# Performance work log

Hardware: AMD Instinct MI355X
Metric: run time of the kernel (lower is better)

Reference implementation:

```python
import jax, jax.numpy as jnp
import numpy as np

N_NODES = 100000
N_EDGES = 1600000
D_FEAT = 128


def setup_inputs() -> dict:
    key = jax.random.key(0)
    k1, k2, k3 = jax.random.split(key, 3)
    feat = jax.random.normal(k1, (N_NODES, D_FEAT), dtype=jnp.float32)
    src = jax.random.randint(k2, (N_EDGES,), 0, N_NODES, dtype=jnp.int32)
    dst = jax.random.randint(k3, (N_EDGES,), 0, N_NODES, dtype=jnp.int32)
    return {"feat": feat, "src": src, "dst": dst}


def reference(feat, src, dst):
    # DGL update_all(copy_src('h','m'), mean('m','neigh')):
    # gather src features along edges, segment-sum into dst, divide by in-degree.
    msgs = feat[src]  # [E, D] gather
    neigh_sum = jax.ops.segment_sum(msgs, dst, num_segments=N_NODES)  # [N, D]
    deg = jax.ops.segment_sum(jnp.ones((src.shape[0],), dtype=feat.dtype), dst,
                              num_segments=N_NODES)  # [N]
    # DGL mean yields 0 for zero in-degree nodes; clamp denominator to 1.
    h_neigh = neigh_sum / jnp.maximum(deg, 1.0)[:, None]
    return h_neigh
```

## Files before the change

### kernel.cpp

```cpp
#include <hip/hip_runtime.h>

#define N_NODES 100000
#define N_EDGES 1600000
#define D_FEAT  128

#define NBUCK   ((N_NODES + 255) >> 8)
#define CAP     8192


__global__ void k1_coarse_hist(const int* __restrict__ dst,
                               int* __restrict__ ghist) {
    __shared__ int lh[NBUCK];
    for (int t = threadIdx.x; t < NBUCK; t += blockDim.x) lh[t] = 0;
    __syncthreads();
    const size_t total4 = N_EDGES / 4;
    size_t tid    = (size_t)blockIdx.x * blockDim.x + threadIdx.x;
    size_t stride = (size_t)gridDim.x * blockDim.x;
    for (size_t i = tid; i < total4; i += stride) {
        int4 d4 = reinterpret_cast<const int4*>(dst)[i];
        atomicAdd(&lh[d4.x >> 8], 1);
        atomicAdd(&lh[d4.y >> 8], 1);
        atomicAdd(&lh[d4.z >> 8], 1);
        atomicAdd(&lh[d4.w >> 8], 1);
    }
    __syncthreads();
    for (int t = threadIdx.x; t < NBUCK; t += blockDim.x)
        if (lh[t]) atomicAdd(&ghist[t], lh[t]);
}

__global__ void k2_scan(const int* __restrict__ ghist,
                        int* __restrict__ base,
                        int* __restrict__ gcursor) {
    __shared__ int ls[512];
    const int t = threadIdx.x;
    int v = (t < NBUCK) ? ghist[t] : 0;
    ls[t] = v;
    __syncthreads();
    int x = v;
    for (int off = 1; off < 512; off <<= 1) {
        int y = (t >= off) ? ls[t - off] : 0;
        __syncthreads();
        x += y;
        ls[t] = x;
        __syncthreads();
    }
    if (t < NBUCK) {
        base[t]    = x - v;
        gcursor[t] = x - v;
    }
}

__global__ void k3_bucket(const int* __restrict__ src,
                          const int* __restrict__ dst,
                          int* __restrict__ gcursor,
                          int* __restrict__ packed) {
    __shared__ int lh[NBUCK];
    __shared__ int lcur[NBUCK];
    const int total4  = N_EDGES / 4;
    const int chunk4  = (total4 + gridDim.x - 1) / gridDim.x;
    const int start4  = blockIdx.x * chunk4;
    const int end4    = min(total4, start4 + chunk4);

    for (int t = threadIdx.x; t < NBUCK; t += blockDim.x) lh[t] = 0;
    __syncthreads();
    for (int i = start4 + threadIdx.x; i < end4; i += blockDim.x) {
        int4 d4 = reinterpret_cast<const int4*>(dst)[i];
        atomicAdd(&lh[d4.x >> 8], 1);
        atomicAdd(&lh[d4.y >> 8], 1);
        atomicAdd(&lh[d4.z >> 8], 1);
        atomicAdd(&lh[d4.w >> 8], 1);
    }
    __syncthreads();
    for (int t = threadIdx.x; t < NBUCK; t += blockDim.x)
        lcur[t] = lh[t] ? atomicAdd(&gcursor[t], lh[t]) : 0;
    __syncthreads();
    for (int i = start4 + threadIdx.x; i < end4; i += blockDim.x) {
        int4 d4 = reinterpret_cast<const int4*>(dst)[i];
        int4 s4 = reinterpret_cast<const int4*>(src)[i];
        int slot;
        slot = atomicAdd(&lcur[d4.x >> 8], 1);
        packed[slot] = s4.x | ((d4.x & 255) << 17);
        slot = atomicAdd(&lcur[d4.y >> 8], 1);
        packed[slot] = s4.y | ((d4.y & 255) << 17);
        slot = atomicAdd(&lcur[d4.z >> 8], 1);
        packed[slot] = s4.z | ((d4.z & 255) << 17);
        slot = atomicAdd(&lcur[d4.w >> 8], 1);
        packed[slot] = s4.w | ((d4.w & 255) << 17);
    }
}

__global__ void __launch_bounds__(256)
k4_fine(const int* __restrict__ ghist,
        const int* __restrict__ base,
        int* __restrict__ packed,
        int* __restrict__ deg,
        int* __restrict__ offs) {
    __shared__ int lpk[CAP];
    __shared__ int lcnt[256];
    __shared__ int lscan[256];
    __shared__ int lcur[256];
    const int b  = blockIdx.x;
    const int t  = threadIdx.x;
    const int gb = base[b];
    int nb = ghist[b];
    if (nb > CAP) nb = CAP;

    lcnt[t] = 0;
    __syncthreads();
    for (int idx = t; idx < nb; idx += 256) {
        const int p = packed[gb + idx];
        lpk[idx] = p;
        atomicAdd(&lcnt[(p >> 17) & 255], 1);
    }
    __syncthreads();
    lscan[t] = lcnt[t];
    __syncthreads();
    int x = lcnt[t];
    for (int off = 1; off < 256; off <<= 1) {
        int y = (t >= off) ? lscan[t - off] : 0;
        __syncthreads();
        x += y;
        lscan[t] = x;
        __syncthreads();
    }
    const int excl = x - lcnt[t];
    const int node = (b << 8) + t;
    if (node < N_NODES) {
        deg[node]  = lcnt[t];
        offs[node] = gb + excl;
    }
    lcur[t] = excl;
    __syncthreads();
    for (int idx = t; idx < nb; idx += 256) {
        const int p    = lpk[idx];
        const int slot = atomicAdd(&lcur[(p >> 17) & 255], 1);
        packed[gb + slot] = p & 0x1FFFF;
    }
}

__global__ void __launch_bounds__(256)
aggregate(const float* __restrict__ feat,
          const int*   __restrict__ edge_list,
          const int*   __restrict__ offs,
          const int*   __restrict__ deg,
          float*       __restrict__ out) {
    const size_t gtid = (size_t)blockIdx.x * blockDim.x + threadIdx.x;
    const int node = (int)(gtid >> 5);
    const int lane = threadIdx.x & 31;
    if (node >= N_NODES) return;

    const int base = offs[node];
    const int d    = deg[node];
    const size_t col = (size_t)lane * 4;

    float4 acc0 = make_float4(0.f, 0.f, 0.f, 0.f);
    float4 acc1 = make_float4(0.f, 0.f, 0.f, 0.f);
    float4 acc2 = make_float4(0.f, 0.f, 0.f, 0.f);
    float4 acc3 = make_float4(0.f, 0.f, 0.f, 0.f);

    int j = 0;
    for (; j + 3 < d; j += 4) {
        const int s0 = edge_list[base + j];
        const int s1 = edge_list[base + j + 1];
        const int s2 = edge_list[base + j + 2];
        const int s3 = edge_list[base + j + 3];
        float4 a = *reinterpret_cast<const float4*>(feat + (size_t)s0 * D_FEAT + col);
        float4 b = *reinterpret_cast<const float4*>(feat + (size_t)s1 * D_FEAT + col);
        float4 c = *reinterpret_cast<const float4*>(feat + (size_t)s2 * D_FEAT + col);
        float4 e = *reinterpret_cast<const float4*>(feat + (size_t)s3 * D_FEAT + col);
        acc0.x += a.x; acc0.y += a.y; acc0.z += a.z; acc0.w += a.w;
        acc1.x += b.x; acc1.y += b.y; acc1.z += b.z; acc1.w += b.w;
        acc2.x += c.x; acc2.y += c.y; acc2.z += c.z; acc2.w += c.w;
        acc3.x += e.x; acc3.y += e.y; acc3.z += e.z; acc3.w += e.w;
    }
    for (; j < d; ++j) {
        const int s0 = edge_list[base + j];
        float4 a = *reinterpret_cast<const float4*>(feat + (size_t)s0 * D_FEAT + col);
        acc0.x += a.x; acc0.y += a.y; acc0.z += a.z; acc0.w += a.w;
    }
    const float inv = 1.0f / (float)max(d, 1);
    float4 r;
    r.x = (acc0.x + acc1.x + acc2.x + acc3.x) * inv;
    r.y = (acc0.y + acc1.y + acc2.y + acc3.y) * inv;
    r.z = (acc0.z + acc1.z + acc2.z + acc3.z) * inv;
    r.w = (acc0.w + acc1.w + acc2.w + acc3.w) * inv;
    *reinterpret_cast<float4*>(out + (size_t)node * D_FEAT + col) = r;
}

__global__ void zero_out_deg(float* __restrict__ out, float* __restrict__ deg) {
    const size_t total4 = (size_t)N_NODES * D_FEAT / 4;
    size_t tid    = (size_t)blockIdx.x * blockDim.x + threadIdx.x;
    size_t stride = (size_t)gridDim.x * blockDim.x;
    float4 z = make_float4(0.f, 0.f, 0.f, 0.f);
    for (size_t i = tid; i < total4; i += stride)
        reinterpret_cast<float4*>(out)[i] = z;
    for (size_t i = tid; i < N_NODES; i += stride)
        deg[i] = 0.f;
}

__global__ void scatter_atomic(const float* __restrict__ feat,
                               const int*   __restrict__ src,
                               const int*   __restrict__ dst,
                               float*       __restrict__ out,
                               float*       __restrict__ deg) {
    const size_t total  = (size_t)N_EDGES * 32;
    size_t tid    = (size_t)blockIdx.x * blockDim.x + threadIdx.x;
    size_t stride = (size_t)gridDim.x * blockDim.x;
    for (size_t i = tid; i < total; i += stride) {
        const int e = (int)(i >> 5);
        const int c = (int)(i & 31);
        const int s = src[e];
        const int d = dst[e];
        float4 v = reinterpret_cast<const float4*>(feat + (size_t)s * D_FEAT)[c];
        float* o = out + (size_t)d * D_FEAT + (size_t)c * 4;
        unsafeAtomicAdd(o + 0, v.x);
        unsafeAtomicAdd(o + 1, v.y);
        unsafeAtomicAdd(o + 2, v.z);
        unsafeAtomicAdd(o + 3, v.w);
        if (c == 0) unsafeAtomicAdd(deg + d, 1.0f);
    }
}

__global__ void div_mean(float* __restrict__ out, const float* __restrict__ deg) {
    const size_t total4 = (size_t)N_NODES * D_FEAT / 4;
    size_t tid    = (size_t)blockIdx.x * blockDim.x + threadIdx.x;
    size_t stride = (size_t)gridDim.x * blockDim.x;
    for (size_t i = tid; i < total4; i += stride) {
        const float inv = 1.0f / fmaxf(deg[i >> 5], 1.0f);
        float4 v = reinterpret_cast<float4*>(out)[i];
        v.x *= inv; v.y *= inv; v.z *= inv; v.w *= inv;
        reinterpret_cast<float4*>(out)[i] = v;
    }
}

extern "C" void kernel_launch(void* const* d_in, const int* in_sizes, int n_in,
                              void* d_out, int out_size, void* d_ws, size_t ws_size,
                              hipStream_t stream) {
    const float* feat = (const float*)d_in[0];
    const int*   src  = (const int*)d_in[1];
    const int*   dst  = (const int*)d_in[2];
    float* out = (float*)d_out;

    const size_t need = ((size_t)1536 + 2 * N_NODES + N_EDGES) * sizeof(int);

    if (ws_size >= need) {
        int* ghist   = (int*)d_ws;
        int* base    = ghist   + 512;
        int* gcursor = base    + 512;
        int* deg     = gcursor + 512;
        int* offs    = deg     + N_NODES;
        int* packed  = offs    + N_NODES;

        hipMemsetAsync(ghist, 0, NBUCK * sizeof(int), stream);
        k1_coarse_hist<<<256,   256, 0, stream>>>(dst, ghist);
        k2_scan       <<<1,     512, 0, stream>>>(ghist, base, gcursor);
        k3_bucket     <<<256,   256, 0, stream>>>(src, dst, gcursor, packed);
        k4_fine       <<<NBUCK, 256, 0, stream>>>(ghist, base, packed, deg, offs);
        aggregate     <<<12500, 256, 0, stream>>>(feat, packed, offs, deg, out);
    } else {
        float* fdeg = (float*)d_ws;
        zero_out_deg  <<<2048, 256, 0, stream>>>(out, fdeg);
        scatter_atomic<<<8192, 256, 0, stream>>>(feat, src, dst, out, fdeg);
        div_mean      <<<2048, 256, 0, stream>>>(out, fdeg);
    }
}
```

Baseline: 252.0 us.

## Stage bucketed edges in LDS before global scatter; unroll aggregate gather by eight

The bucketing kernel now uses a fixed chunk per block and does a local counting sort of its edges into shared memory, keyed by coarse bucket. It then writes each bucket's run contiguously to global memory, replacing scattered single-word stores with mostly contiguous writes. The aggregate kernel raises its unroll from four to eight independent gathers per step to put more loads in flight. The costs are roughly 50KB of LDS per block in k3, which limits occupancy, and higher register pressure in aggregate.

New measurement: 244.2 us. -3.1%, faster.

```diff
diff --git a/kernel.cpp b/kernel.cpp
--- a/kernel.cpp
+++ b/kernel.cpp
@@ -6,6 +6,8 @@
 
 #define NBUCK   ((N_NODES + 255) >> 8)
 #define CAP     8192
+#define CHUNK4  ((N_EDGES / 4 + 255) / 256)
+#define KCAP    (CHUNK4 * 4)
 
 
 __global__ void k1_coarse_hist(const int* __restrict__ dst,
@@ -50,20 +52,28 @@
     }
 }
 
-__global__ void k3_bucket(const int* __restrict__ src,
-                          const int* __restrict__ dst,
-                          int* __restrict__ gcursor,
-                          int* __restrict__ packed) {
-    __shared__ int lh[NBUCK];
+__global__ void __launch_bounds__(256)
+k3_bucket(const int* __restrict__ src,
+          const int* __restrict__ dst,
+          int* __restrict__ gcursor,
+          int* __restrict__ packed) {
+    __shared__ int lh[512];
+    __shared__ int lstart[512];
+    __shared__ int lbase[NBUCK];
     __shared__ int lcur[NBUCK];
-    const int total4  = N_EDGES / 4;
-    const int chunk4  = (total4 + gridDim.x - 1) / gridDim.x;
-    const int start4  = blockIdx.x * chunk4;
-    const int end4    = min(total4, start4 + chunk4);
-
-    for (int t = threadIdx.x; t < NBUCK; t += blockDim.x) lh[t] = 0;
-    __syncthreads();
-    for (int i = start4 + threadIdx.x; i < end4; i += blockDim.x) {
+    __shared__ int lscan[256];
+    __shared__ int sortv[KCAP];
+    __shared__ unsigned short sortb[KCAP];
+
+    const int total4 = N_EDGES / 4;
+    const int start4 = blockIdx.x * CHUNK4;
+    const int end4   = min(total4, start4 + CHUNK4);
+    const int t      = threadIdx.x;
+
+    for (int i = t; i < 512; i += 256) lh[i] = 0;
+    for (int i = t; i < NBUCK; i += 256) lcur[i] = 0;
+    __syncthreads();
+    for (int i = start4 + t; i < end4; i += 256) {
         int4 d4 = reinterpret_cast<const int4*>(dst)[i];
         atomicAdd(&lh[d4.x >> 8], 1);
         atomicAdd(&lh[d4.y >> 8], 1);
@@ -71,21 +81,43 @@
         atomicAdd(&lh[d4.w >> 8], 1);
     }
     __syncthreads();
-    for (int t = threadIdx.x; t < NBUCK; t += blockDim.x)
-        lcur[t] = lh[t] ? atomicAdd(&gcursor[t], lh[t]) : 0;
-    __syncthreads();
-    for (int i = start4 + threadIdx.x; i < end4; i += blockDim.x) {
+    const int v0 = lh[2 * t], v1 = lh[2 * t + 1];
+    const int s  = v0 + v1;
+    lscan[t] = s;
+    __syncthreads();
+    int x = s;
+    for (int off = 1; off < 256; off <<= 1) {
+        int y = (t >= off) ? lscan[t - off] : 0;
+        __syncthreads();
+        x += y;
+        lscan[t] = x;
+        __syncthreads();
+    }
+    lstart[2 * t]     = x - s;
+    lstart[2 * t + 1] = x - s + v0;
+    for (int b = t; b < NBUCK; b += 256) {
+        const int c = lh[b];
+        lbase[b] = c ? atomicAdd(&gcursor[b], c) : 0;
+    }
+    __syncthreads();
+    for (int i = start4 + t; i < end4; i += 256) {
         int4 d4 = reinterpret_cast<const int4*>(dst)[i];
         int4 s4 = reinterpret_cast<const int4*>(src)[i];
-        int slot;
-        slot = atomicAdd(&lcur[d4.x >> 8], 1);
-        packed[slot] = s4.x | ((d4.x & 255) << 17);
-        slot = atomicAdd(&lcur[d4.y >> 8], 1);
-        packed[slot] = s4.y | ((d4.y & 255) << 17);
-        slot = atomicAdd(&lcur[d4.z >> 8], 1);
-        packed[slot] = s4.z | ((d4.z & 255) << 17);
-        slot = atomicAdd(&lcur[d4.w >> 8], 1);
-        packed[slot] = s4.w | ((d4.w & 255) << 17);
+        int b, sl;
+        b = d4.x >> 8; sl = lstart[b] + atomicAdd(&lcur[b], 1);
+        sortv[sl] = s4.x | ((d4.x & 255) << 17); sortb[sl] = (unsigned short)b;
+        b = d4.y >> 8; sl = lstart[b] + atomicAdd(&lcur[b], 1);
+        sortv[sl] = s4.y | ((d4.y & 255) << 17); sortb[sl] = (unsigned short)b;
+        b = d4.z >> 8; sl = lstart[b] + atomicAdd(&lcur[b], 1);
+        sortv[sl] = s4.z | ((d4.z & 255) << 17); sortb[sl] = (unsigned short)b;
+        b = d4.w >> 8; sl = lstart[b] + atomicAdd(&lcur[b], 1);
+        sortv[sl] = s4.w | ((d4.w & 255) << 17); sortb[sl] = (unsigned short)b;
+    }
+    __syncthreads();
+    const int n = (end4 - start4) * 4;
+    for (int j = t; j < n; j += 256) {
+        const int b = sortb[j];
+        packed[lbase[b] + (j - lstart[b])] = sortv[j];
     }
 }
 
@@ -153,37 +185,41 @@
     const int d    = deg[node];
     const size_t col = (size_t)lane * 4;
 
-    float4 acc0 = make_float4(0.f, 0.f, 0.f, 0.f);
-    float4 acc1 = make_float4(0.f, 0.f, 0.f, 0.f);
-    float4 acc2 = make_float4(0.f, 0.f, 0.f, 0.f);
-    float4 acc3 = make_float4(0.f, 0.f, 0.f, 0.f);
+    float4 acc[8];
+    #pragma unroll
+    for (int k = 0; k < 8; ++k) acc[k] = make_float4(0.f, 0.f, 0.f, 0.f);
 
     int j = 0;
-    for (; j + 3 < d; j += 4) {
-        const int s0 = edge_list[base + j];
-        const int s1 = edge_list[base + j + 1];
-        const int s2 = edge_list[base + j + 2];
-        const int s3 = edge_list[base + j + 3];
-        float4 a = *reinterpret_cast<const float4*>(feat + (size_t)s0 * D_FEAT + col);
-        float4 b = *reinterpret_cast<const float4*>(feat + (size_t)s1 * D_FEAT + col);
-        float4 c = *reinterpret_cast<const float4*>(feat + (size_t)s2 * D_FEAT + col);
-        float4 e = *reinterpret_cast<const float4*>(feat + (size_t)s3 * D_FEAT + col);
-        acc0.x += a.x; acc0.y += a.y; acc0.z += a.z; acc0.w += a.w;
-        acc1.x += b.x; acc1.y += b.y; acc1.z += b.z; acc1.w += b.w;
-        acc2.x += c.x; acc2.y += c.y; acc2.z += c.z; acc2.w += c.w;
-        acc3.x += e.x; acc3.y += e.y; acc3.z += e.z; acc3.w += e.w;
+    for (; j + 7 < d; j += 8) {
+        int sid[8];
+        #pragma unroll
+        for (int k = 0; k < 8; ++k) sid[k] = edge_list[base + j + k];
+        float4 f[8];
+        #pragma unroll
+        for (int k = 0; k < 8; ++k)
+            f[k] = *reinterpret_cast<const float4*>(
+                feat + (size_t)sid[k] * D_FEAT + col);
+        #pragma unroll
+        for (int k = 0; k < 8; ++k) {
+            acc[k].x += f[k].x; acc[k].y += f[k].y;
+            acc[k].z += f[k].z; acc[k].w += f[k].w;
+        }
     }
     for (; j < d; ++j) {
         const int s0 = edge_list[base + j];
-        float4 a = *reinterpret_cast<const float4*>(feat + (size_t)s0 * D_FEAT + col);
-        acc0.x += a.x; acc0.y += a.y; acc0.z += a.z; acc0.w += a.w;
+        const float4 a = *reinterpret_cast<const float4*>(
+            feat + (size_t)s0 * D_FEAT + col);
+        acc[0].x += a.x; acc[0].y += a.y; acc[0].z += a.z; acc[0].w += a.w;
+    }
+    #pragma unroll
+    for (int k = 1; k < 8; ++k) {
+        acc[0].x += acc[k].x; acc[0].y += acc[k].y;
+        acc[0].z += acc[k].z; acc[0].w += acc[k].w;
     }
     const float inv = 1.0f / (float)max(d, 1);
     float4 r;
-    r.x = (acc0.x + acc1.x + acc2.x + acc3.x) * inv;
-    r.y = (acc0.y + acc1.y + acc2.y + acc3.y) * inv;
-    r.z = (acc0.z + acc1.z + acc2.z + acc3.z) * inv;
-    r.w = (acc0.w + acc1.w + acc2.w + acc3.w) * inv;
+    r.x = acc[0].x * inv; r.y = acc[0].y * inv;
+    r.z = acc[0].z * inv; r.w = acc[0].w * inv;
     *reinterpret_cast<float4*>(out + (size_t)node * D_FEAT + col) = r;
 }
 
```
